# Performance work log

Hardware: AMD Instinct MI355X
Metric: run time of the kernel (lower is better)

The kernel has to match this reference:

```python
import jax, jax.numpy as jnp
import numpy as np

D_MODEL = 512
NUM_HEADS = 8
D_K = D_MODEL // NUM_HEADS


def setup_inputs() -> dict:
    key = jax.random.key(0)
    k0, k1, k2, k3, k4 = jax.random.split(key, 5)
    s = 1.0 / np.sqrt(D_MODEL)
    return {
        "x": jax.random.normal(k0, (2, 4096, D_MODEL), dtype=jnp.float32),
        "W_q": jax.random.normal(k1, (D_MODEL, D_MODEL), dtype=jnp.float32) * s,
        "W_k": jax.random.normal(k2, (D_MODEL, D_MODEL), dtype=jnp.float32) * s,
        "W_v": jax.random.normal(k3, (D_MODEL, D_MODEL), dtype=jnp.float32) * s,
        "W_o": jax.random.normal(k4, (D_MODEL, D_MODEL), dtype=jnp.float32) * s,
    }


def reference(x, W_q, W_k, W_v, W_o):
    B, S, _ = x.shape
    # project and split heads: (B, H, S, d_k)
    def split(t):
        return t.reshape(B, S, NUM_HEADS, D_K).transpose(0, 2, 1, 3)
    Q = split(x @ W_q)
    K = split(x @ W_k)
    V = split(x @ W_v)
    scale = jnp.sqrt(jnp.asarray(D_K, dtype=x.dtype))
    logits = jnp.einsum('bhqd,bhkd->bhqk', Q, K) / scale
    attn = jax.nn.softmax(logits, axis=-1)  # dropout is identity at inference
    out = jnp.einsum('bhqk,bhkd->bhqd', attn, V)
    concat = out.transpose(0, 2, 1, 3).reshape(B, S, D_MODEL)
    return concat @ W_o
```

## Files before the change

### kernel.cpp

```cpp
#include <hip/hip_runtime.h>
#include <hip/hip_bf16.h>


#define DMODEL 512
#define SEQ    4096
#define NTOK   8192
#define LDQK   1024

using f32x4 = __attribute__((ext_vector_type(4))) float;
using s16x8 = __attribute__((ext_vector_type(8))) short;
using u16x8 = __attribute__((ext_vector_type(8))) unsigned short;

static __device__ __forceinline__ unsigned short f2bf(float f) {
  union { float f; unsigned u; } v; v.f = f;
  unsigned r = v.u + 0x7fff + ((v.u >> 16) & 1);
  return (unsigned short)(r >> 16);
}

static __device__ __forceinline__ unsigned pack_bf2(float lo, float hi) {
  __hip_bfloat162 t = __float22bfloat162_rn(make_float2(lo, hi));
  union { __hip_bfloat162 b; unsigned u; } c; c.b = t; return c.u;
}

static __device__ __forceinline__ void gll16(const void* g, void* l) {
  __builtin_amdgcn_global_load_lds(
      (const __attribute__((address_space(1))) unsigned int*)g,
      (__attribute__((address_space(3))) unsigned int*)l, 16, 0, 0);
}

__global__ void cast_x_kernel(const float* __restrict__ x,
                              unsigned short* __restrict__ xb, int n4) {
  int i = blockIdx.x * blockDim.x + threadIdx.x;
  if (i >= n4) return;
  float4 v = ((const float4*)x)[i];
  ushort4 o;
  o.x = f2bf(v.x); o.y = f2bf(v.y); o.z = f2bf(v.z); o.w = f2bf(v.w);
  ((ushort4*)xb)[i] = o;
}

__global__ void wtrans4_kernel(const float* __restrict__ Wq,
                               const float* __restrict__ Wk,
                               const float* __restrict__ Wv,
                               const float* __restrict__ Wo,
                               unsigned short* __restrict__ Wall, float c2) {
  int y = blockIdx.y;
  int idx = blockIdx.x * 256 + threadIdx.x;
  const float* W = (y == 0) ? Wq : (y == 1) ? Wk : (y == 2) ? Wv : Wo;
  float scale = (y == 0) ? c2 : 1.0f;
  int k = idx & 511, n = idx >> 9;
  Wall[y * 262144 + idx] = f2bf(W[k * 512 + n] * scale);
}

__global__ __launch_bounds__(256, 3) void gemm_qkv(
    const unsigned short* __restrict__ xb,
    const unsigned short* __restrict__ Wall,
    unsigned short* __restrict__ QKb,
    unsigned short* __restrict__ Vtb)
{
  __shared__ unsigned short As[128 * 32];
  __shared__ unsigned short Bs[128 * 32];
  const int by = blockIdx.y;
  const bool vmode = (by >= 8);
  const unsigned short* A  = vmode ? (Wall + 2 * 262144) : xb;
  const unsigned short* Bt = vmode ? xb : Wall;
  const size_t bm = vmode ? (size_t)(by - 8) * 128 : (size_t)blockIdx.x * 128;
  const size_t bn = vmode ? (size_t)blockIdx.x * 128 : (size_t)by * 128;
  const int tid  = threadIdx.x;
  const int wave = tid >> 6, lane = tid & 63;
  const int q4 = lane >> 4, ln = lane & 15;
  const int wm = (wave >> 1) * 64, wn = (wave & 1) * 64;
  f32x4 acc[4][4] = {};
  const int srow = wave * 16 + (lane >> 2);
  const int scol = (lane & 3) * 8;

  const unsigned short* Ag  = A  + (bm + srow)      * 512 + scol;
  const unsigned short* Ag2 = A  + (bm + 64 + srow) * 512 + scol;
  const unsigned short* Bg  = Bt + (bn + srow)      * 512 + scol;
  const unsigned short* Bg2 = Bt + (bn + 64 + srow) * 512 + scol;
  unsigned short* Ad  = As + wave * 512;
  unsigned short* Ad2 = As + 2048 + wave * 512;
  unsigned short* Bd  = Bs + wave * 512;
  unsigned short* Bd2 = Bs + 2048 + wave * 512;

  for (int kt = 0; kt < 512; kt += 32) {
    __syncthreads();
    gll16(Ag + kt,  Ad);
    gll16(Ag2 + kt, Ad2);
    gll16(Bg + kt,  Bd);
    gll16(Bg2 + kt, Bd2);
    __syncthreads();
    s16x8 af[4], bfr[4];
#pragma unroll
    for (int i = 0; i < 4; i++)
      af[i] = *(const s16x8*)(As + (wm + i * 16 + ln) * 32 + q4 * 8);
#pragma unroll
    for (int i = 0; i < 4; i++)
      bfr[i] = *(const s16x8*)(Bs + (wn + i * 16 + ln) * 32 + q4 * 8);
#pragma unroll
    for (int mi = 0; mi < 4; mi++)
#pragma unroll
      for (int ni = 0; ni < 4; ni++)
        acc[mi][ni] = __builtin_amdgcn_mfma_f32_16x16x32_bf16(
            af[mi], bfr[ni], acc[mi][ni], 0, 0, 0);
  }
#pragma unroll
  for (int mi = 0; mi < 4; mi++)
#pragma unroll
    for (int r = 0; r < 4; ++r) {
      size_t row = bm + wm + mi * 16 + q4 * 4 + r;
#pragma unroll
      for (int ni = 0; ni < 4; ni++) {
        size_t col = bn + wn + ni * 16 + ln;
        unsigned short hv = f2bf(acc[mi][ni][r]);
        if (!vmode) {
          QKb[row * 1024 + col] = hv;
        } else {
          int b = (int)(col >> 12), s = (int)(col & 4095);
          int sp = (s & ~63) | (s & 32) | (((s >> 2) & 3) << 3) |
                   (((s >> 4) & 1) << 2) | (s & 3);
          Vtb[(size_t)b * 2097152 + row * 4096 + sp] = hv;
        }
      }
    }
}

__global__ __launch_bounds__(256, 2) void attn_kernel(
    const unsigned short* __restrict__ QK,
    const unsigned short* __restrict__ Vt,
    unsigned short* __restrict__ Oc)
{
  const int qt = blockIdx.x, h = blockIdx.y, b = blockIdx.z;
  const int tid = threadIdx.x, wave = tid >> 6, lane = tid & 63;
  const int q4 = lane >> 4, ln = lane & 15;
  __shared__ unsigned short Ks[2][64 * 72];
  __shared__ unsigned short Vs[2][64 * 72];
  const size_t rowbase = (size_t)b * SEQ;
  const size_t qrow0   = (size_t)qt * 128 + wave * 32;
  const unsigned short* Kp  = QK + rowbase * LDQK + 512 + h * 64;
  const unsigned short* VTp = Vt + ((size_t)(b * 8 + h) * 64) * SEQ;

  s16x8 qf[2][2];
#pragma unroll
  for (int mf = 0; mf < 2; ++mf) {
    const unsigned short* q = QK + (rowbase + qrow0 + mf * 16 + ln) * LDQK + h * 64;
    qf[mf][0] = *(const s16x8*)(q + q4 * 8);
    qf[mf][1] = *(const s16x8*)(q + 32 + q4 * 8);
  }
  f32x4 o[2][4] = {};
  float lp[2] = {};

  const int srow = tid >> 2;
  const int scol = (tid & 3) * 16;

  const unsigned short* kgp = Kp  + (size_t)srow * LDQK + scol;
  const unsigned short* vgp = VTp + (size_t)srow * SEQ  + scol;

  u16x8 kr  = *(const u16x8*)kgp;
  u16x8 kr2 = *(const u16x8*)(kgp + 8);
  u16x8 vr  = *(const u16x8*)vgp;
  u16x8 vr2 = *(const u16x8*)(vgp + 8);
  *(u16x8*)(Ks[0] + srow * 72 + scol)     = kr;
  *(u16x8*)(Ks[0] + srow * 72 + scol + 8) = kr2;
  *(u16x8*)(Vs[0] + srow * 72 + scol)     = vr;
  *(u16x8*)(Vs[0] + srow * 72 + scol + 8) = vr2;
  kgp += (size_t)64 * LDQK;  vgp += 64;
  kr  = *(const u16x8*)kgp;
  kr2 = *(const u16x8*)(kgp + 8);
  vr  = *(const u16x8*)vgp;
  vr2 = *(const u16x8*)(vgp + 8);
  __syncthreads();

  for (int t = 0; t < SEQ / 64; ++t) {
    const int cur = t & 1;
    const unsigned short* Kc = Ks[cur];
    const unsigned short* Vc = Vs[cur];

    f32x4 s4[2][4] = {};
#pragma unroll
    for (int ni = 0; ni < 4; ni++) {
      const unsigned short* kb = Kc + (ni * 16 + ln) * 72 + q4 * 8;
      s16x8 kf0 = *(const s16x8*)kb;
      s16x8 kf1 = *(const s16x8*)(kb + 32);
#pragma unroll
      for (int mf = 0; mf < 2; ++mf) {
        s4[mf][ni] = __builtin_amdgcn_mfma_f32_16x16x32_bf16(kf0, qf[mf][0], s4[mf][ni], 0, 0, 0);
        s4[mf][ni] = __builtin_amdgcn_mfma_f32_16x16x32_bf16(kf1, qf[mf][1], s4[mf][ni], 0, 0, 0);
      }
    }
    s16x8 vf[2][4];
#pragma unroll
    for (int ks = 0; ks < 2; ++ks)
#pragma unroll
      for (int ni = 0; ni < 4; ni++)
        vf[ks][ni] = *(const s16x8*)(Vc + (ni * 16 + ln) * 72 + ks * 32 + q4 * 8);

    s16x8 pf[2][2];
#pragma unroll
    for (int mf = 0; mf < 2; ++mf) {
      float e[4][4];
      float ls = 0.f;
#pragma unroll
      for (int ni = 0; ni < 4; ni++)
#pragma unroll
        for (int r = 0; r < 4; ++r) {
          e[ni][r] = __builtin_amdgcn_exp2f(s4[mf][ni][r]);
          ls += e[ni][r];
        }
      lp[mf] += ls;
#pragma unroll
      for (int ks = 0; ks < 2; ++ks) {
        union { s16x8 v; unsigned u[4]; } pu;
        pu.u[0] = pack_bf2(e[2 * ks][0],     e[2 * ks][1]);
        pu.u[1] = pack_bf2(e[2 * ks][2],     e[2 * ks][3]);
        pu.u[2] = pack_bf2(e[2 * ks + 1][0], e[2 * ks + 1][1]);
        pu.u[3] = pack_bf2(e[2 * ks + 1][2], e[2 * ks + 1][3]);
        pf[mf][ks] = pu.v;
      }
    }
#pragma unroll
    for (int ks = 0; ks < 2; ++ks)
#pragma unroll
      for (int ni = 0; ni < 4; ni++)
#pragma unroll
        for (int mf = 0; mf < 2; ++mf)
          o[mf][ni] = __builtin_amdgcn_mfma_f32_16x16x32_bf16(pf[mf][ks], vf[ks][ni], o[mf][ni], 0, 0, 0);

    if (t + 1 < SEQ / 64) {
      unsigned short* Kn = Ks[cur ^ 1];
      unsigned short* Vn = Vs[cur ^ 1];
      *(u16x8*)(Kn + srow * 72 + scol)     = kr;
      *(u16x8*)(Kn + srow * 72 + scol + 8) = kr2;
      *(u16x8*)(Vn + srow * 72 + scol)     = vr;
      *(u16x8*)(Vn + srow * 72 + scol + 8) = vr2;
      if (t + 2 < SEQ / 64) {
        kgp += (size_t)64 * LDQK;  vgp += 64;
        kr  = *(const u16x8*)kgp;
        kr2 = *(const u16x8*)(kgp + 8);
        vr  = *(const u16x8*)vgp;
        vr2 = *(const u16x8*)(vgp + 8);
      }
    }
    __syncthreads();
  }
#pragma unroll
  for (int mf = 0; mf < 2; ++mf) {
    float l = lp[mf];
    l += __shfl_xor(l, 16, 64);
    l += __shfl_xor(l, 32, 64);
    lp[mf] = l;
  }
#pragma unroll
  for (int mf = 0; mf < 2; ++mf)
#pragma unroll
    for (int r = 0; r < 4; ++r) {
      float lv = __shfl(lp[mf], q4 * 4 + r, 64);
      float inv = 1.0f / lv;
      size_t row = rowbase + qrow0 + mf * 16 + q4 * 4 + r;
#pragma unroll
      for (int ni = 0; ni < 4; ni++)
        Oc[row * DMODEL + h * 64 + ni * 16 + ln] = f2bf(o[mf][ni][r] * inv);
    }
}

__global__ __launch_bounds__(256, 3) void gemm_out(
    const unsigned short* __restrict__ A,
    const unsigned short* __restrict__ Bt,
    float* __restrict__ C)
{
  __shared__ unsigned short As[128 * 32];
  __shared__ unsigned short Bs[64 * 32];
  const int tid  = threadIdx.x;
  const int wave = tid >> 6, lane = tid & 63;
  const int q4 = lane >> 4, ln = lane & 15;
  const size_t bm = (size_t)blockIdx.x * 128;
  const size_t bn = (size_t)blockIdx.y * 64;
  const int wm = (wave >> 1) * 64, wn = (wave & 1) * 32;
  f32x4 acc[4][2] = {};
  const int srow = wave * 16 + (lane >> 2);
  const int scol = (lane & 3) * 8;

  const unsigned short* Ag  = A  + (bm + srow)      * 512 + scol;
  const unsigned short* Ag2 = A  + (bm + 64 + srow) * 512 + scol;
  const unsigned short* Bg  = Bt + (bn + srow)      * 512 + scol;
  unsigned short* Ad  = As + wave * 512;
  unsigned short* Ad2 = As + 2048 + wave * 512;
  unsigned short* Bd  = Bs + wave * 512;

  for (int kt = 0; kt < 512; kt += 32) {
    __syncthreads();
    gll16(Ag + kt,  Ad);
    gll16(Ag2 + kt, Ad2);
    gll16(Bg + kt,  Bd);
    __syncthreads();
    s16x8 af[4], bfr[2];
#pragma unroll
    for (int i = 0; i < 4; i++)
      af[i] = *(const s16x8*)(As + (wm + i * 16 + ln) * 32 + q4 * 8);
#pragma unroll
    for (int i = 0; i < 2; i++)
      bfr[i] = *(const s16x8*)(Bs + (wn + i * 16 + ln) * 32 + q4 * 8);
#pragma unroll
    for (int mi = 0; mi < 4; mi++)
#pragma unroll
      for (int ni = 0; ni < 2; ni++)
        acc[mi][ni] = __builtin_amdgcn_mfma_f32_16x16x32_bf16(
            af[mi], bfr[ni], acc[mi][ni], 0, 0, 0);
  }
#pragma unroll
  for (int mi = 0; mi < 4; mi++)
#pragma unroll
    for (int r = 0; r < 4; ++r) {
      size_t row = bm + wm + mi * 16 + q4 * 4 + r;
#pragma unroll
      for (int ni = 0; ni < 2; ni++)
        C[row * 512 + bn + wn + ni * 16 + ln] = acc[mi][ni][r];
    }
}

extern "C" void kernel_launch(void* const* d_in, const int* in_sizes, int n_in,
                              void* d_out, int out_size, void* d_ws, size_t ws_size,
                              hipStream_t stream) {
  const float* x  = (const float*)d_in[0];
  const float* Wq = (const float*)d_in[1];
  const float* Wk = (const float*)d_in[2];
  const float* Wv = (const float*)d_in[3];
  const float* Wo = (const float*)d_in[4];

  char* ws = (char*)d_ws;
  unsigned short* xb   = (unsigned short*)(ws);
  unsigned short* Wall = (unsigned short*)(ws + 8388608);
  unsigned short* QKb  = (unsigned short*)(ws + 10485760);
  unsigned short* Vtb  = (unsigned short*)(ws + 27262976);
  unsigned short* Oc   = (unsigned short*)(ws + 35651584);

  const float C2 = 0.125f * 1.44269504088896f;

  hipLaunchKernelGGL(cast_x_kernel, dim3(NTOK * DMODEL / 4 / 256), dim3(256), 0,
                     stream, x, xb, NTOK * DMODEL / 4);
  hipLaunchKernelGGL(wtrans4_kernel, dim3(1024, 4), dim3(256), 0, stream,
                     Wq, Wk, Wv, Wo, Wall, C2);
  hipLaunchKernelGGL(gemm_qkv, dim3(64, 12), dim3(256), 0, stream,
                     xb, Wall, QKb, Vtb);
  hipLaunchKernelGGL(attn_kernel, dim3(32, 8, 2), dim3(256), 0, stream,
                     QKb, Vtb, Oc);
  hipLaunchKernelGGL(gemm_out, dim3(64, 8), dim3(256), 0, stream,
                     Oc, Wall + 3 * 262144, (float*)d_out);
}
```

Measured before the change: 195.6 us.

## Split attention key tile across wave pairs and tile weight transpose via LDS

The attention kernel now assigns each pair of waves 64 query rows and splits each 64-key tile between them, so every wave holds 4 query fragments and reuses each K/V fragment read from LDS across more MFMAs. The partial outputs and row sums from the two key halves are combined through shared memory at the end. This adds a reduction step and more accumulator registers per wave. Separately, the weight transpose/cast kernel now uses a 64x64 LDS tile so that both its global reads and its writes are coalesced, replacing strided per-element reads.

```diff
diff --git a/kernel.cpp b/kernel.cpp
--- a/kernel.cpp
+++ b/kernel.cpp
@@ -43,12 +43,33 @@
                                const float* __restrict__ Wv,
                                const float* __restrict__ Wo,
                                unsigned short* __restrict__ Wall, float c2) {
-  int y = blockIdx.y;
-  int idx = blockIdx.x * 256 + threadIdx.x;
+  __shared__ float T[64][65];
+  const int y = blockIdx.y;
   const float* W = (y == 0) ? Wq : (y == 1) ? Wk : (y == 2) ? Wv : Wo;
-  float scale = (y == 0) ? c2 : 1.0f;
-  int k = idx & 511, n = idx >> 9;
-  Wall[y * 262144 + idx] = f2bf(W[k * 512 + n] * scale);
+  const float scale = (y == 0) ? c2 : 1.0f;
+  const int tk = (blockIdx.x & 7) * 64;
+  const int tn = (blockIdx.x >> 3) * 64;
+  const int r  = threadIdx.x >> 2;
+  const int cq = threadIdx.x & 3;
+#pragma unroll
+  for (int i = 0; i < 4; ++i) {
+    int c = (cq + 4 * i) * 4;
+    float4 v = *(const float4*)&W[(size_t)(tk + r) * 512 + tn + c];
+    T[r][c + 0] = v.x * scale; T[r][c + 1] = v.y * scale;
+    T[r][c + 2] = v.z * scale; T[r][c + 3] = v.w * scale;
+  }
+  __syncthreads();
+  const int n  = threadIdx.x >> 2;
+  const int k0 = (threadIdx.x & 3) * 16;
+#pragma unroll
+  for (int j4 = 0; j4 < 4; ++j4) {
+    ushort4 o;
+    o.x = f2bf(T[k0 + j4 * 4 + 0][n]);
+    o.y = f2bf(T[k0 + j4 * 4 + 1][n]);
+    o.z = f2bf(T[k0 + j4 * 4 + 2][n]);
+    o.w = f2bf(T[k0 + j4 * 4 + 3][n]);
+    *(ushort4*)&Wall[(size_t)y * 262144 + (size_t)(tn + n) * 512 + tk + k0 + j4 * 4] = o;
+  }
 }
 
 __global__ __launch_bounds__(256, 3) void gemm_qkv(
@@ -132,22 +153,24 @@
   const int qt = blockIdx.x, h = blockIdx.y, b = blockIdx.z;
   const int tid = threadIdx.x, wave = tid >> 6, lane = tid & 63;
   const int q4 = lane >> 4, ln = lane & 15;
-  __shared__ unsigned short Ks[2][64 * 72];
-  __shared__ unsigned short Vs[2][64 * 72];
+  const int wq = wave >> 1, wk = wave & 1;
+  __shared__ __align__(16) unsigned char SM[36864];
+  unsigned short* KsB = (unsigned short*)SM;
+  unsigned short* VsB = (unsigned short*)(SM + 18432);
   const size_t rowbase = (size_t)b * SEQ;
-  const size_t qrow0   = (size_t)qt * 128 + wave * 32;
+  const size_t qrow0   = (size_t)qt * 128 + wq * 64;
   const unsigned short* Kp  = QK + rowbase * LDQK + 512 + h * 64;
   const unsigned short* VTp = Vt + ((size_t)(b * 8 + h) * 64) * SEQ;
 
-  s16x8 qf[2][2];
-#pragma unroll
-  for (int mf = 0; mf < 2; ++mf) {
-    const unsigned short* q = QK + (rowbase + qrow0 + mf * 16 + ln) * LDQK + h * 64;
-    qf[mf][0] = *(const s16x8*)(q + q4 * 8);
-    qf[mf][1] = *(const s16x8*)(q + 32 + q4 * 8);
-  }
-  f32x4 o[2][4] = {};
-  float lp[2] = {};
+  s16x8 qf[4][2];
+#pragma unroll
+  for (int nt = 0; nt < 4; ++nt) {
+    const unsigned short* q = QK + (rowbase + qrow0 + nt * 16 + ln) * LDQK + h * 64;
+    qf[nt][0] = *(const s16x8*)(q + q4 * 8);
+    qf[nt][1] = *(const s16x8*)(q + 32 + q4 * 8);
+  }
+  f32x4 o[4][4] = {};
+  float lp[4] = {};
 
   const int srow = tid >> 2;
   const int scol = (tid & 3) * 16;
@@ -159,10 +182,10 @@
   u16x8 kr2 = *(const u16x8*)(kgp + 8);
   u16x8 vr  = *(const u16x8*)vgp;
   u16x8 vr2 = *(const u16x8*)(vgp + 8);
-  *(u16x8*)(Ks[0] + srow * 72 + scol)     = kr;
-  *(u16x8*)(Ks[0] + srow * 72 + scol + 8) = kr2;
-  *(u16x8*)(Vs[0] + srow * 72 + scol)     = vr;
-  *(u16x8*)(Vs[0] + srow * 72 + scol + 8) = vr2;
+  *(u16x8*)(KsB + srow * 72 + scol)     = kr;
+  *(u16x8*)(KsB + srow * 72 + scol + 8) = kr2;
+  *(u16x8*)(VsB + srow * 72 + scol)     = vr;
+  *(u16x8*)(VsB + srow * 72 + scol + 8) = vr2;
   kgp += (size_t)64 * LDQK;  vgp += 64;
   kr  = *(const u16x8*)kgp;
   kr2 = *(const u16x8*)(kgp + 8);
@@ -172,62 +195,52 @@
 
   for (int t = 0; t < SEQ / 64; ++t) {
     const int cur = t & 1;
-    const unsigned short* Kc = Ks[cur];
-    const unsigned short* Vc = Vs[cur];
+    const unsigned short* Kc = KsB + cur * 4608;
+    const unsigned short* Vc = VsB + cur * 4608;
 
     f32x4 s4[2][4] = {};
 #pragma unroll
-    for (int ni = 0; ni < 4; ni++) {
-      const unsigned short* kb = Kc + (ni * 16 + ln) * 72 + q4 * 8;
-      s16x8 kf0 = *(const s16x8*)kb;
-      s16x8 kf1 = *(const s16x8*)(kb + 32);
-#pragma unroll
-      for (int mf = 0; mf < 2; ++mf) {
-        s4[mf][ni] = __builtin_amdgcn_mfma_f32_16x16x32_bf16(kf0, qf[mf][0], s4[mf][ni], 0, 0, 0);
-        s4[mf][ni] = __builtin_amdgcn_mfma_f32_16x16x32_bf16(kf1, qf[mf][1], s4[mf][ni], 0, 0, 0);
+    for (int mi = 0; mi < 2; ++mi)
+#pragma unroll
+      for (int c = 0; c < 2; ++c) {
+        s16x8 kf = *(const s16x8*)(Kc + (wk * 32 + mi * 16 + ln) * 72 + c * 32 + q4 * 8);
+#pragma unroll
+        for (int nt = 0; nt < 4; ++nt)
+          s4[mi][nt] = __builtin_amdgcn_mfma_f32_16x16x32_bf16(kf, qf[nt][c], s4[mi][nt], 0, 0, 0);
       }
-    }
-    s16x8 vf[2][4];
-#pragma unroll
-    for (int ks = 0; ks < 2; ++ks)
-#pragma unroll
-      for (int ni = 0; ni < 4; ni++)
-        vf[ks][ni] = *(const s16x8*)(Vc + (ni * 16 + ln) * 72 + ks * 32 + q4 * 8);
-
-    s16x8 pf[2][2];
-#pragma unroll
-    for (int mf = 0; mf < 2; ++mf) {
-      float e[4][4];
-      float ls = 0.f;
-#pragma unroll
-      for (int ni = 0; ni < 4; ni++)
-#pragma unroll
-        for (int r = 0; r < 4; ++r) {
-          e[ni][r] = __builtin_amdgcn_exp2f(s4[mf][ni][r]);
-          ls += e[ni][r];
-        }
-      lp[mf] += ls;
-#pragma unroll
-      for (int ks = 0; ks < 2; ++ks) {
-        union { s16x8 v; unsigned u[4]; } pu;
-        pu.u[0] = pack_bf2(e[2 * ks][0],     e[2 * ks][1]);
-        pu.u[1] = pack_bf2(e[2 * ks][2],     e[2 * ks][3]);
-        pu.u[2] = pack_bf2(e[2 * ks + 1][0], e[2 * ks + 1][1]);
-        pu.u[3] = pack_bf2(e[2 * ks + 1][2], e[2 * ks + 1][3]);
-        pf[mf][ks] = pu.v;
-      }
-    }
-#pragma unroll
-    for (int ks = 0; ks < 2; ++ks)
-#pragma unroll
-      for (int ni = 0; ni < 4; ni++)
-#pragma unroll
-        for (int mf = 0; mf < 2; ++mf)
-          o[mf][ni] = __builtin_amdgcn_mfma_f32_16x16x32_bf16(pf[mf][ks], vf[ks][ni], o[mf][ni], 0, 0, 0);
+    s16x8 vf[4];
+#pragma unroll
+    for (int dt = 0; dt < 4; ++dt)
+      vf[dt] = *(const s16x8*)(Vc + (dt * 16 + ln) * 72 + wk * 32 + q4 * 8);
+
+    s16x8 pf[4];
+#pragma unroll
+    for (int nt = 0; nt < 4; ++nt) {
+      float e00 = __builtin_amdgcn_exp2f(s4[0][nt][0]);
+      float e01 = __builtin_amdgcn_exp2f(s4[0][nt][1]);
+      float e02 = __builtin_amdgcn_exp2f(s4[0][nt][2]);
+      float e03 = __builtin_amdgcn_exp2f(s4[0][nt][3]);
+      float e10 = __builtin_amdgcn_exp2f(s4[1][nt][0]);
+      float e11 = __builtin_amdgcn_exp2f(s4[1][nt][1]);
+      float e12 = __builtin_amdgcn_exp2f(s4[1][nt][2]);
+      float e13 = __builtin_amdgcn_exp2f(s4[1][nt][3]);
+      lp[nt] += ((e00 + e01) + (e02 + e03)) + ((e10 + e11) + (e12 + e13));
+      union { s16x8 v; unsigned u[4]; } pu;
+      pu.u[0] = pack_bf2(e00, e01);
+      pu.u[1] = pack_bf2(e02, e03);
+      pu.u[2] = pack_bf2(e10, e11);
+      pu.u[3] = pack_bf2(e12, e13);
+      pf[nt] = pu.v;
+    }
+#pragma unroll
+    for (int nt = 0; nt < 4; ++nt)
+#pragma unroll
+      for (int dt = 0; dt < 4; ++dt)
+        o[nt][dt] = __builtin_amdgcn_mfma_f32_16x16x32_bf16(pf[nt], vf[dt], o[nt][dt], 0, 0, 0);
 
     if (t + 1 < SEQ / 64) {
-      unsigned short* Kn = Ks[cur ^ 1];
-      unsigned short* Vn = Vs[cur ^ 1];
+      unsigned short* Kn = KsB + (cur ^ 1) * 4608;
+      unsigned short* Vn = VsB + (cur ^ 1) * 4608;
       *(u16x8*)(Kn + srow * 72 + scol)     = kr;
       *(u16x8*)(Kn + srow * 72 + scol + 8) = kr2;
       *(u16x8*)(Vn + srow * 72 + scol)     = vr;
@@ -242,24 +255,44 @@
     }
     __syncthreads();
   }
-#pragma unroll
-  for (int mf = 0; mf < 2; ++mf) {
-    float l = lp[mf];
-    l += __shfl_xor(l, 16, 64);
-    l += __shfl_xor(l, 32, 64);
-    lp[mf] = l;
-  }
-#pragma unroll
-  for (int mf = 0; mf < 2; ++mf)
-#pragma unroll
-    for (int r = 0; r < 4; ++r) {
-      float lv = __shfl(lp[mf], q4 * 4 + r, 64);
-      float inv = 1.0f / lv;
-      size_t row = rowbase + qrow0 + mf * 16 + q4 * 4 + r;
-#pragma unroll
-      for (int ni = 0; ni < 4; ni++)
-        Oc[row * DMODEL + h * 64 + ni * 16 + ln] = f2bf(o[mf][ni][r] * inv);
-    }
+
+#pragma unroll
+  for (int nt = 0; nt < 4; ++nt) {
+    lp[nt] += __shfl_xor(lp[nt], 16, 64);
+    lp[nt] += __shfl_xor(lp[nt], 32, 64);
+  }
+  float* Red  = (float*)SM;
+  float* RedL = (float*)(SM + 32768);
+  if (wk == 1) {
+#pragma unroll
+    for (int nt = 0; nt < 4; ++nt) {
+#pragma unroll
+      for (int dt = 0; dt < 4; ++dt)
+        *(f32x4*)(Red + ((wq * 16 + nt * 4 + dt) * 64 + lane) * 4) = o[nt][dt];
+      RedL[(wq * 4 + nt) * 64 + lane] = lp[nt];
+    }
+  }
+  __syncthreads();
+  if (wk == 0) {
+#pragma unroll
+    for (int nt = 0; nt < 4; ++nt) {
+#pragma unroll
+      for (int dt = 0; dt < 4; ++dt)
+        o[nt][dt] += *(const f32x4*)(Red + ((wq * 16 + nt * 4 + dt) * 64 + lane) * 4);
+      lp[nt] += RedL[(wq * 4 + nt) * 64 + lane];
+    }
+#pragma unroll
+    for (int nt = 0; nt < 4; ++nt)
+#pragma unroll
+      for (int r = 0; r < 4; ++r) {
+        float lv = __shfl(lp[nt], q4 * 4 + r, 64);
+        float inv = 1.0f / lv;
+        size_t row = rowbase + qrow0 + nt * 16 + q4 * 4 + r;
+#pragma unroll
+        for (int dt = 0; dt < 4; ++dt)
+          Oc[row * DMODEL + h * 64 + dt * 16 + ln] = f2bf(o[nt][dt][r] * inv);
+      }
+  }
 }
 
 __global__ __launch_bounds__(256, 3) void gemm_out(
@@ -337,7 +370,7 @@
 
   hipLaunchKernelGGL(cast_x_kernel, dim3(NTOK * DMODEL / 4 / 256), dim3(256), 0,
                      stream, x, xb, NTOK * DMODEL / 4);
-  hipLaunchKernelGGL(wtrans4_kernel, dim3(1024, 4), dim3(256), 0, stream,
+  hipLaunchKernelGGL(wtrans4_kernel, dim3(64, 4), dim3(256), 0, stream,
                      Wq, Wk, Wv, Wo, Wall, C2);
   hipLaunchKernelGGL(gemm_qkv, dim3(64, 12), dim3(256), 0, stream,
                      xb, Wall, QKb, Vtb);
```

Measured after the change: 192.5 us. Within noise of the previous version (-1.6%).

## Split attention over two key chunks and merge partials inside output GEMM

Applied to the files above, without the earlier changes.

The attention kernel now splits the key sequence into two halves across the grid z dimension, which doubles the block count to fill more compute units. It writes unnormalized fp32 partial outputs and row sums. The output projection GEMM sums the two partials, normalizes, converts to bf16 and stages the result in LDS instead of loading precomputed bf16. The x cast and weight transpose are also fused into one prep kernel, with the transpose done through an LDS tile for coalesced access. The split relies on a fixed max (exp2 without running max subtraction, implied by the merge), and it adds extra fp32 traffic of about 32MB written plus read.

```diff
diff --git a/kernel.cpp b/kernel.cpp
--- a/kernel.cpp
+++ b/kernel.cpp
@@ -28,27 +28,51 @@
       (__attribute__((address_space(3))) unsigned int*)l, 16, 0, 0);
 }
 
-__global__ void cast_x_kernel(const float* __restrict__ x,
-                              unsigned short* __restrict__ xb, int n4) {
-  int i = blockIdx.x * blockDim.x + threadIdx.x;
-  if (i >= n4) return;
-  float4 v = ((const float4*)x)[i];
-  ushort4 o;
-  o.x = f2bf(v.x); o.y = f2bf(v.y); o.z = f2bf(v.z); o.w = f2bf(v.w);
-  ((ushort4*)xb)[i] = o;
-}
-
-__global__ void wtrans4_kernel(const float* __restrict__ Wq,
-                               const float* __restrict__ Wk,
-                               const float* __restrict__ Wv,
-                               const float* __restrict__ Wo,
-                               unsigned short* __restrict__ Wall, float c2) {
-  int y = blockIdx.y;
-  int idx = blockIdx.x * 256 + threadIdx.x;
+__global__ void prep_kernel(const float* __restrict__ x,
+                            const float* __restrict__ Wq,
+                            const float* __restrict__ Wk,
+                            const float* __restrict__ Wv,
+                            const float* __restrict__ Wo,
+                            unsigned short* __restrict__ xb,
+                            unsigned short* __restrict__ Wall, float c2) {
+  __shared__ float T[64][65];
+  const int bx = blockIdx.x;
+  if (bx < 1024) {
+    for (int i = bx * 256 + threadIdx.x; i < NTOK * DMODEL / 4; i += 262144) {
+      float4 v = ((const float4*)x)[i];
+      ushort4 o;
+      o.x = f2bf(v.x); o.y = f2bf(v.y); o.z = f2bf(v.z); o.w = f2bf(v.w);
+      ((ushort4*)xb)[i] = o;
+    }
+    return;
+  }
+  const int t = bx - 1024;
+  const int y = t >> 6, sub = t & 63;
   const float* W = (y == 0) ? Wq : (y == 1) ? Wk : (y == 2) ? Wv : Wo;
-  float scale = (y == 0) ? c2 : 1.0f;
-  int k = idx & 511, n = idx >> 9;
-  Wall[y * 262144 + idx] = f2bf(W[k * 512 + n] * scale);
+  const float scale = (y == 0) ? c2 : 1.0f;
+  const int tk = (sub & 7) * 64;
+  const int tn = (sub >> 3) * 64;
+  const int r  = threadIdx.x >> 2;
+  const int cq = threadIdx.x & 3;
+#pragma unroll
+  for (int i = 0; i < 4; ++i) {
+    int c = (cq + 4 * i) * 4;
+    float4 v = *(const float4*)&W[(size_t)(tk + r) * 512 + tn + c];
+    T[r][c + 0] = v.x * scale; T[r][c + 1] = v.y * scale;
+    T[r][c + 2] = v.z * scale; T[r][c + 3] = v.w * scale;
+  }
+  __syncthreads();
+  const int n  = threadIdx.x >> 2;
+  const int k0 = (threadIdx.x & 3) * 16;
+#pragma unroll
+  for (int j4 = 0; j4 < 4; ++j4) {
+    ushort4 o;
+    o.x = f2bf(T[k0 + j4 * 4 + 0][n]);
+    o.y = f2bf(T[k0 + j4 * 4 + 1][n]);
+    o.z = f2bf(T[k0 + j4 * 4 + 2][n]);
+    o.w = f2bf(T[k0 + j4 * 4 + 3][n]);
+    *(ushort4*)&Wall[(size_t)y * 262144 + (size_t)(tn + n) * 512 + tk + k0 + j4 * 4] = o;
+  }
 }
 
 __global__ __launch_bounds__(256, 3) void gemm_qkv(
@@ -127,9 +151,11 @@
 __global__ __launch_bounds__(256, 2) void attn_kernel(
     const unsigned short* __restrict__ QK,
     const unsigned short* __restrict__ Vt,
-    unsigned short* __restrict__ Oc)
+    float* __restrict__ Opart,
+    float* __restrict__ Lpart)
 {
-  const int qt = blockIdx.x, h = blockIdx.y, b = blockIdx.z;
+  const int qt = blockIdx.x, h = blockIdx.y, z = blockIdx.z;
+  const int b = z >> 1, ck = z & 1;
   const int tid = threadIdx.x, wave = tid >> 6, lane = tid & 63;
   const int q4 = lane >> 4, ln = lane & 15;
   __shared__ unsigned short Ks[2][64 * 72];
@@ -152,8 +178,8 @@
   const int srow = tid >> 2;
   const int scol = (tid & 3) * 16;
 
-  const unsigned short* kgp = Kp  + (size_t)srow * LDQK + scol;
-  const unsigned short* vgp = VTp + (size_t)srow * SEQ  + scol;
+  const unsigned short* kgp = Kp  + (size_t)(ck * 2048 + srow) * LDQK + scol;
+  const unsigned short* vgp = VTp + (size_t)srow * SEQ + ck * 2048 + scol;
 
   u16x8 kr  = *(const u16x8*)kgp;
   u16x8 kr2 = *(const u16x8*)(kgp + 8);
@@ -170,7 +196,7 @@
   vr2 = *(const u16x8*)(vgp + 8);
   __syncthreads();
 
-  for (int t = 0; t < SEQ / 64; ++t) {
+  for (int t = 0; t < 32; ++t) {
     const int cur = t & 1;
     const unsigned short* Kc = Ks[cur];
     const unsigned short* Vc = Vs[cur];
@@ -225,14 +251,14 @@
         for (int mf = 0; mf < 2; ++mf)
           o[mf][ni] = __builtin_amdgcn_mfma_f32_16x16x32_bf16(pf[mf][ks], vf[ks][ni], o[mf][ni], 0, 0, 0);
 
-    if (t + 1 < SEQ / 64) {
+    if (t + 1 < 32) {
       unsigned short* Kn = Ks[cur ^ 1];
       unsigned short* Vn = Vs[cur ^ 1];
       *(u16x8*)(Kn + srow * 72 + scol)     = kr;
       *(u16x8*)(Kn + srow * 72 + scol + 8) = kr2;
       *(u16x8*)(Vn + srow * 72 + scol)     = vr;
       *(u16x8*)(Vn + srow * 72 + scol + 8) = vr2;
-      if (t + 2 < SEQ / 64) {
+      if (t + 2 < 32) {
         kgp += (size_t)64 * LDQK;  vgp += 64;
         kr  = *(const u16x8*)kgp;
         kr2 = *(const u16x8*)(kgp + 8);
@@ -247,23 +273,24 @@
     float l = lp[mf];
     l += __shfl_xor(l, 16, 64);
     l += __shfl_xor(l, 32, 64);
-    lp[mf] = l;
-  }
+    if (q4 == 0)
+      Lpart[(size_t)ck * 65536 + (size_t)(b * 8 + h) * 4096 + qrow0 + mf * 16 + ln] = l;
+  }
+  float* Opc = Opart + (size_t)ck * NTOK * DMODEL;
 #pragma unroll
   for (int mf = 0; mf < 2; ++mf)
 #pragma unroll
     for (int r = 0; r < 4; ++r) {
-      float lv = __shfl(lp[mf], q4 * 4 + r, 64);
-      float inv = 1.0f / lv;
       size_t row = rowbase + qrow0 + mf * 16 + q4 * 4 + r;
 #pragma unroll
       for (int ni = 0; ni < 4; ni++)
-        Oc[row * DMODEL + h * 64 + ni * 16 + ln] = f2bf(o[mf][ni][r] * inv);
-    }
-}
-
-__global__ __launch_bounds__(256, 3) void gemm_out(
-    const unsigned short* __restrict__ A,
+        Opc[row * DMODEL + h * 64 + ni * 16 + ln] = o[mf][ni][r];
+    }
+}
+
+__global__ __launch_bounds__(256, 2) void gemm_out(
+    const float* __restrict__ Opart,
+    const float* __restrict__ Lpart,
     const unsigned short* __restrict__ Bt,
     float* __restrict__ C)
 {
@@ -279,18 +306,53 @@
   const int srow = wave * 16 + (lane >> 2);
   const int scol = (lane & 3) * 8;
 
-  const unsigned short* Ag  = A  + (bm + srow)      * 512 + scol;
-  const unsigned short* Ag2 = A  + (bm + 64 + srow) * 512 + scol;
-  const unsigned short* Bg  = Bt + (bn + srow)      * 512 + scol;
-  unsigned short* Ad  = As + wave * 512;
-  unsigned short* Ad2 = As + 2048 + wave * 512;
-  unsigned short* Bd  = Bs + wave * 512;
+  const size_t r0 = bm + srow, r1 = bm + 64 + srow;
+  float invA[8], invB[8];
+  {
+    const size_t q0 = r0 & 4095, b0 = r0 >> 12;
+    const size_t q1 = r1 & 4095, b1 = r1 >> 12;
+#pragma unroll
+    for (int hh = 0; hh < 8; ++hh) {
+      invA[hh] = 1.0f / (Lpart[(b0 * 8 + hh) * 4096 + q0] +
+                         Lpart[65536 + (b0 * 8 + hh) * 4096 + q0]);
+      invB[hh] = 1.0f / (Lpart[(b1 * 8 + hh) * 4096 + q1] +
+                         Lpart[65536 + (b1 * 8 + hh) * 4096 + q1]);
+    }
+  }
+  const float* A0a = Opart + r0 * 512;
+  const float* A0b = Opart + (size_t)NTOK * DMODEL + r0 * 512;
+  const float* A1a = Opart + r1 * 512;
+  const float* A1b = Opart + (size_t)NTOK * DMODEL + r1 * 512;
+  const unsigned short* Bg = Bt + (bn + srow) * 512 + scol;
+  unsigned short* Bd = Bs + wave * 512;
 
   for (int kt = 0; kt < 512; kt += 32) {
     __syncthreads();
-    gll16(Ag + kt,  Ad);
-    gll16(Ag2 + kt, Ad2);
-    gll16(Bg + kt,  Bd);
+    gll16(Bg + kt, Bd);
+    const int c0 = kt + scol;
+    const int hh = c0 >> 6;
+    {
+      f32x4 xa = *(const f32x4*)(A0a + c0),  xa2 = *(const f32x4*)(A0a + c0 + 4);
+      f32x4 xb = *(const f32x4*)(A0b + c0),  xb2 = *(const f32x4*)(A0b + c0 + 4);
+      float iv = invA[hh];
+      union { u16x8 v; unsigned u[4]; } pu;
+      pu.u[0] = pack_bf2((xa[0] + xb[0]) * iv, (xa[1] + xb[1]) * iv);
+      pu.u[1] = pack_bf2((xa[2] + xb[2]) * iv, (xa[3] + xb[3]) * iv);
+      pu.u[2] = pack_bf2((xa2[0] + xb2[0]) * iv, (xa2[1] + xb2[1]) * iv);
+      pu.u[3] = pack_bf2((xa2[2] + xb2[2]) * iv, (xa2[3] + xb2[3]) * iv);
+      *(u16x8*)(As + srow * 32 + scol) = pu.v;
+    }
+    {
+      f32x4 xa = *(const f32x4*)(A1a + c0),  xa2 = *(const f32x4*)(A1a + c0 + 4);
+      f32x4 xb = *(const f32x4*)(A1b + c0),  xb2 = *(const f32x4*)(A1b + c0 + 4);
+      float iv = invB[hh];
+      union { u16x8 v; unsigned u[4]; } pu;
+      pu.u[0] = pack_bf2((xa[0] + xb[0]) * iv, (xa[1] + xb[1]) * iv);
+      pu.u[1] = pack_bf2((xa[2] + xb[2]) * iv, (xa[3] + xb[3]) * iv);
+      pu.u[2] = pack_bf2((xa2[0] + xb2[0]) * iv, (xa2[1] + xb2[1]) * iv);
+      pu.u[3] = pack_bf2((xa2[2] + xb2[2]) * iv, (xa2[3] + xb2[3]) * iv);
+      *(u16x8*)(As + (64 + srow) * 32 + scol) = pu.v;
+    }
     __syncthreads();
     s16x8 af[4], bfr[2];
 #pragma unroll
@@ -327,22 +389,21 @@
   const float* Wo = (const float*)d_in[4];
 
   char* ws = (char*)d_ws;
-  unsigned short* xb   = (unsigned short*)(ws);
-  unsigned short* Wall = (unsigned short*)(ws + 8388608);
-  unsigned short* QKb  = (unsigned short*)(ws + 10485760);
-  unsigned short* Vtb  = (unsigned short*)(ws + 27262976);
-  unsigned short* Oc   = (unsigned short*)(ws + 35651584);
+  unsigned short* xb    = (unsigned short*)(ws);
+  unsigned short* Wall  = (unsigned short*)(ws + 8388608);
+  unsigned short* QKb   = (unsigned short*)(ws + 10485760);
+  unsigned short* Vtb   = (unsigned short*)(ws + 27262976);
+  float*          Opart = (float*)(ws + 35651584);
+  float*          Lpart = (float*)(ws + 69206016);
 
   const float C2 = 0.125f * 1.44269504088896f;
 
-  hipLaunchKernelGGL(cast_x_kernel, dim3(NTOK * DMODEL / 4 / 256), dim3(256), 0,
-                     stream, x, xb, NTOK * DMODEL / 4);
-  hipLaunchKernelGGL(wtrans4_kernel, dim3(1024, 4), dim3(256), 0, stream,
-                     Wq, Wk, Wv, Wo, Wall, C2);
+  hipLaunchKernelGGL(prep_kernel, dim3(1280), dim3(256), 0, stream,
+                     x, Wq, Wk, Wv, Wo, xb, Wall, C2);
   hipLaunchKernelGGL(gemm_qkv, dim3(64, 12), dim3(256), 0, stream,
                      xb, Wall, QKb, Vtb);
-  hipLaunchKernelGGL(attn_kernel, dim3(32, 8, 2), dim3(256), 0, stream,
-                     QKb, Vtb, Oc);
+  hipLaunchKernelGGL(attn_kernel, dim3(32, 8, 4), dim3(256), 0, stream,
+                     QKb, Vtb, Opart, Lpart);
   hipLaunchKernelGGL(gemm_out, dim3(64, 8), dim3(256), 0, stream,
-                     Oc, Wall + 3 * 262144, (float*)d_out);
-}
+                     Opart, Lpart, Wall + 3 * 262144, (float*)d_out);
+}
```

Result: no change. 199.5 us (+2.0%).
